# Optimization experiments

Hardware: AMD Instinct MI355X
Metric: run time of the kernel (lower is better)

## Reference

```python
import jax, jax.numpy as jnp
import numpy as np

N_NODES = 50000
N_EDGES = 800000
D_IN = 64
D_OUT = 64

def setup_inputs() -> dict:
    key = jax.random.key(0)
    k1, k2, k3, k4 = jax.random.split(key, 4)
    x = jax.random.normal(k1, (N_NODES, D_IN), dtype=jnp.float32)
    # Linear(in, out, bias=False): weight shape [out, in], Kaiming-uniform-ish scale
    bound = 1.0 / np.sqrt(D_IN)
    W = jax.random.uniform(k2, (D_OUT, D_IN), dtype=jnp.float32, minval=-bound, maxval=bound)
    src = jax.random.randint(k3, (N_EDGES,), 0, N_NODES, dtype=jnp.int32)
    dst = jax.random.randint(k4, (N_EDGES,), 0, N_NODES, dtype=jnp.int32)
    return {"x": x, "W": W, "src": src, "dst": dst}

def reference(x, W, src, dst):
    # update_all(copy_src, sum): for each edge (s, d), add x[s] into node d
    agg = jax.ops.segment_sum(x[src], dst, num_segments=N_NODES)  # [N, D_IN]
    # linear1 (bias=False); dropout is identity at inference
    h = jnp.einsum('nd,od->no', agg, W)  # [N, D_OUT]
    h = jax.nn.relu(h)
    # is_normalize=False -> skip L2 normalize; residual adds input node features
    return h + x
```

## Files before the change

kernel.cpp:

```cpp
#include <hip/hip_runtime.h>

#define D 64
#define NCHUNK 256
#define GEMMB 1024
#define CAP 48

__device__ __forceinline__ float bflo(unsigned u) { return __uint_as_float(u << 16); }
__device__ __forceinline__ float bfhi(unsigned u) { return __uint_as_float(u & 0xffff0000u); }
__device__ __forceinline__ unsigned short f2bf(float f) {
    unsigned b = __float_as_uint(f);
    return (unsigned short)((b + 0x7fffu + ((b >> 16) & 1u)) >> 16);
}

__global__ __launch_bounds__(256) void hist_kernel(
    const int* __restrict__ dst, unsigned int* __restrict__ bh32, int n_nodes, int ne) {
    __shared__ unsigned int lds[12544];
    const int tid = threadIdx.x;
    const int nw = (n_nodes + 3) >> 2;
    const int c = blockIdx.x;
    const int csz = (ne + NCHUNK - 1) / NCHUNK;
    const int e0 = c * csz, e1 = min(e0 + csz, ne);
    for (int i = tid; i < nw; i += 256) lds[i] = 0;
    __syncthreads();
    for (int e = e0 + tid; e < e1; e += 256) {
        const int d = dst[e];
        atomicAdd(&lds[d >> 2], 1u << ((d & 3) * 8));
    }
    __syncthreads();
    unsigned int* bh = bh32 + (size_t)c * nw;
    for (int i = tid; i < nw; i += 256) bh[i] = lds[i];
}

__global__ __launch_bounds__(256) void colscan_gemm_kernel(
    const float* __restrict__ x, const float* __restrict__ W,
    unsigned char* __restrict__ bh8, int* __restrict__ counts,
    unsigned short* __restrict__ ybf, int n_nodes, int ne, int csb) {
    __shared__ float lds[5184];
    const int tid = threadIdx.x;
    if ((int)blockIdx.x < csb) {
        const int d = blockIdx.x * 256 + tid;
        if (d >= n_nodes) return;
        const size_t npad4 = (size_t)((n_nodes + 3) >> 2) * 4;
        int acc = 0;
        for (int c0 = 0; c0 < NCHUNK; c0 += 8) {
            unsigned char v[8];
#pragma unroll
            for (int k = 0; k < 8; ++k) v[k] = bh8[(size_t)(c0 + k) * npad4 + d];
#pragma unroll
            for (int k = 0; k < 8; ++k) {
                bh8[(size_t)(c0 + k) * npad4 + d] = (unsigned char)acc;
                acc += v[k];
            }
        }
        counts[d] = acc;
    } else {
        float* Wt = lds;
        float* As = Wt + 64 * 65;
        for (int i = tid; i < 4096; i += 256) {
            const int o = i >> 6, k = i & 63;
            Wt[k * 65 + o] = W[i];
        }
        const int w = tid >> 6, o = tid & 63;
        const float4* x4 = (const float4*)x;
        const int ngrp = (n_nodes + 15) >> 4;
        for (int grp = blockIdx.x - csb; grp < ngrp; grp += GEMMB) {
            const int base = grp * 16;
            __syncthreads();
            const int idx = base * 16 + tid;
            if (idx < n_nodes * 16) ((float4*)As)[tid] = x4[idx];
            __syncthreads();
            const float* a0 = &As[(w * 4 + 0) * 64];
            const float* a1 = &As[(w * 4 + 1) * 64];
            const float* a2 = &As[(w * 4 + 2) * 64];
            const float* a3 = &As[(w * 4 + 3) * 64];
            float h0 = 0.f, h1 = 0.f, h2 = 0.f, h3 = 0.f;
#pragma unroll
            for (int k = 0; k < 64; ++k) {
                const float wv = Wt[k * 65 + o];
                h0 = fmaf(a0[k], wv, h0);
                h1 = fmaf(a1[k], wv, h1);
                h2 = fmaf(a2[k], wv, h2);
                h3 = fmaf(a3[k], wv, h3);
            }
            const int n0 = base + w * 4;
            if (n0 + 3 < n_nodes) {
                ybf[(size_t)(n0 + 0) * D + o] = f2bf(h0);
                ybf[(size_t)(n0 + 1) * D + o] = f2bf(h1);
                ybf[(size_t)(n0 + 2) * D + o] = f2bf(h2);
                ybf[(size_t)(n0 + 3) * D + o] = f2bf(h3);
            } else {
                if (n0 + 0 < n_nodes) ybf[(size_t)(n0 + 0) * D + o] = f2bf(h0);
                if (n0 + 1 < n_nodes) ybf[(size_t)(n0 + 1) * D + o] = f2bf(h1);
                if (n0 + 2 < n_nodes) ybf[(size_t)(n0 + 2) * D + o] = f2bf(h2);
                if (n0 + 3 < n_nodes) ybf[(size_t)(n0 + 3) * D + o] = f2bf(h3);
            }
        }
    }
}

__global__ __launch_bounds__(256) void place_kernel(
    const int* __restrict__ src, const int* __restrict__ dst,
    const unsigned int* __restrict__ bh32, int* __restrict__ esrc,
    int n_nodes, int ne) {
    __shared__ unsigned int lw[12544];
    const int c = blockIdx.x;
    const int csz = (ne + NCHUNK - 1) / NCHUNK;
    const int e0 = c * csz, e1 = min(e0 + csz, ne);
    const int nw = (n_nodes + 3) >> 2;
    const unsigned int* bh = bh32 + (size_t)c * nw;
    for (int i = threadIdx.x; i < nw; i += 256) lw[i] = bh[i];
    __syncthreads();
    for (int e = e0 + threadIdx.x; e < e1; e += 256) {
        const int d = dst[e];
        const unsigned old = atomicAdd(&lw[d >> 2], 1u << ((d & 3) * 8));
        const int slot = (old >> ((d & 3) * 8)) & 0xff;
        if (slot < CAP) esrc[d * CAP + slot] = src[e];
    }
}

__global__ void gather_kernel(const int* __restrict__ counts, const int* __restrict__ esrc,
                              const unsigned short* __restrict__ ybf,
                              const float* __restrict__ x, float* __restrict__ out,
                              int n_nodes) {
    const int tid = threadIdx.x;
    const int w = tid >> 6, lane = tid & 63;
    const int g = lane >> 3, m = lane & 7;
    const uint4* Y4 = (const uint4*)ybf;
    const float4* x4 = (const float4*)x;
    float4* out4 = (float4*)out;
    const int nWaves = gridDim.x * 4;

    int n = blockIdx.x * 4 + w;
    int c = 0, s_all = 0;
    if (n < n_nodes) {
        c = min(counts[n], CAP);
        s_all = (lane < c) ? esrc[n * CAP + lane] : 0;
    }
    while (n < n_nodes) {
        const int n2 = n + nWaves;
        int c2 = 0, s2 = 0;
        if (n2 < n_nodes) {
            c2 = min(counts[n2], CAP);
            s2 = (lane < c2) ? esrc[n2 * CAP + lane] : 0;
        }
        float acc[8] = {0.f, 0.f, 0.f, 0.f, 0.f, 0.f, 0.f, 0.f};
        for (int j = 0; j < c; j += 8) {
            const int e = j + g;
            const int s = __shfl(s_all, e);
            if (e < c) {
                const uint4 v = Y4[(size_t)s * 8 + m];
                acc[0] += bflo(v.x); acc[1] += bfhi(v.x);
                acc[2] += bflo(v.y); acc[3] += bfhi(v.y);
                acc[4] += bflo(v.z); acc[5] += bfhi(v.z);
                acc[6] += bflo(v.w); acc[7] += bfhi(v.w);
            }
        }
#pragma unroll
        for (int k = 0; k < 8; ++k) {
            acc[k] += __shfl_xor(acc[k], 8);
            acc[k] += __shfl_xor(acc[k], 16);
            acc[k] += __shfl_xor(acc[k], 32);
        }
        if (lane < 8) {
            const float4 xa = x4[(size_t)n * 16 + lane * 2];
            const float4 xb = x4[(size_t)n * 16 + lane * 2 + 1];
            float4 oa, ob;
            oa.x = fmaxf(acc[0], 0.f) + xa.x;
            oa.y = fmaxf(acc[1], 0.f) + xa.y;
            oa.z = fmaxf(acc[2], 0.f) + xa.z;
            oa.w = fmaxf(acc[3], 0.f) + xa.w;
            ob.x = fmaxf(acc[4], 0.f) + xb.x;
            ob.y = fmaxf(acc[5], 0.f) + xb.y;
            ob.z = fmaxf(acc[6], 0.f) + xb.z;
            ob.w = fmaxf(acc[7], 0.f) + xb.w;
            out4[(size_t)n * 16 + lane * 2] = oa;
            out4[(size_t)n * 16 + lane * 2 + 1] = ob;
        }
        n = n2; c = c2; s_all = s2;
    }
}

extern "C" void kernel_launch(void* const* d_in, const int* in_sizes, int n_in,
                              void* d_out, int out_size, void* d_ws, size_t ws_size,
                              hipStream_t stream) {
    const float* x = (const float*)d_in[0];
    const float* W = (const float*)d_in[1];
    const int* src = (const int*)d_in[2];
    const int* dst = (const int*)d_in[3];
    float* out = (float*)d_out;

    const int n_nodes = in_sizes[0] / D;
    const int n_edges = in_sizes[2];
    const int nw = (n_nodes + 3) >> 2;

    unsigned int* bh32 = (unsigned int*)d_ws;
    int* counts = (int*)(bh32 + (size_t)NCHUNK * nw);
    int* esrc = counts + n_nodes;
    unsigned short* ybf = (unsigned short*)(esrc + (size_t)n_nodes * CAP);

    const int csb = (n_nodes + 255) / 256;

    hist_kernel<<<NCHUNK, 256, 0, stream>>>(dst, bh32, n_nodes, n_edges);
    colscan_gemm_kernel<<<csb + GEMMB, 256, 0, stream>>>(
        x, W, (unsigned char*)bh32, counts, ybf, n_nodes, n_edges, csb);
    place_kernel<<<NCHUNK, 256, 0, stream>>>(src, dst, bh32, esrc, n_nodes, n_edges);
    gather_kernel<<<2048, 256, 0, stream>>>(counts, esrc, ybf, x, out, n_nodes);
}
```

Baseline: 136.2 us.

## Replace chunked histogram counting sort with global atomic slot assignment

Removes the per-chunk LDS histogram kernel and the column prefix scan, and replaces them with a zeroing pass fused into the GEMM kernel plus a per-edge global atomicAdd on node counters to pick each edge's bucket slot. This eliminates a kernel launch and the large per-chunk histogram buffer traffic. In exchange, edge order within each node becomes nondeterministic and global atomics may contend on popular nodes.

Result: slower. 153.9 us (+13.0%).

```diff
diff --git a/kernel.cpp b/kernel.cpp
--- a/kernel.cpp
+++ b/kernel.cpp
@@ -1,8 +1,8 @@
 #include <hip/hip_runtime.h>
 
 #define D 64
-#define NCHUNK 256
 #define GEMMB 1024
+#define ZB 32
 #define CAP 48
 
 __device__ __forceinline__ float bflo(unsigned u) { return __uint_as_float(u << 16); }
@@ -12,110 +12,66 @@
     return (unsigned short)((b + 0x7fffu + ((b >> 16) & 1u)) >> 16);
 }
 
-__global__ __launch_bounds__(256) void hist_kernel(
-    const int* __restrict__ dst, unsigned int* __restrict__ bh32, int n_nodes, int ne) {
-    __shared__ unsigned int lds[12544];
-    const int tid = threadIdx.x;
-    const int nw = (n_nodes + 3) >> 2;
-    const int c = blockIdx.x;
-    const int csz = (ne + NCHUNK - 1) / NCHUNK;
-    const int e0 = c * csz, e1 = min(e0 + csz, ne);
-    for (int i = tid; i < nw; i += 256) lds[i] = 0;
-    __syncthreads();
-    for (int e = e0 + tid; e < e1; e += 256) {
-        const int d = dst[e];
-        atomicAdd(&lds[d >> 2], 1u << ((d & 3) * 8));
-    }
-    __syncthreads();
-    unsigned int* bh = bh32 + (size_t)c * nw;
-    for (int i = tid; i < nw; i += 256) bh[i] = lds[i];
-}
-
-__global__ __launch_bounds__(256) void colscan_gemm_kernel(
+__global__ __launch_bounds__(256) void zero_gemm_kernel(
     const float* __restrict__ x, const float* __restrict__ W,
-    unsigned char* __restrict__ bh8, int* __restrict__ counts,
-    unsigned short* __restrict__ ybf, int n_nodes, int ne, int csb) {
+    int* __restrict__ counts, unsigned short* __restrict__ ybf, int n_nodes) {
     __shared__ float lds[5184];
     const int tid = threadIdx.x;
-    if ((int)blockIdx.x < csb) {
-        const int d = blockIdx.x * 256 + tid;
-        if (d >= n_nodes) return;
-        const size_t npad4 = (size_t)((n_nodes + 3) >> 2) * 4;
-        int acc = 0;
-        for (int c0 = 0; c0 < NCHUNK; c0 += 8) {
-            unsigned char v[8];
+    if ((int)blockIdx.x < ZB) {
+        for (int i = blockIdx.x * 256 + tid; i < n_nodes; i += ZB * 256) counts[i] = 0;
+        return;
+    }
+    float* Wt = lds;
+    float* As = Wt + 64 * 65;
+    for (int i = tid; i < 4096; i += 256) {
+        const int o = i >> 6, k = i & 63;
+        Wt[k * 65 + o] = W[i];
+    }
+    const int w = tid >> 6, o = tid & 63;
+    const float4* x4 = (const float4*)x;
+    const int ngrp = (n_nodes + 15) >> 4;
+    for (int grp = blockIdx.x - ZB; grp < ngrp; grp += GEMMB) {
+        const int base = grp * 16;
+        __syncthreads();
+        const int idx = base * 16 + tid;
+        if (idx < n_nodes * 16) ((float4*)As)[tid] = x4[idx];
+        __syncthreads();
+        const float* a0 = &As[(w * 4 + 0) * 64];
+        const float* a1 = &As[(w * 4 + 1) * 64];
+        const float* a2 = &As[(w * 4 + 2) * 64];
+        const float* a3 = &As[(w * 4 + 3) * 64];
+        float h0 = 0.f, h1 = 0.f, h2 = 0.f, h3 = 0.f;
 #pragma unroll
-            for (int k = 0; k < 8; ++k) v[k] = bh8[(size_t)(c0 + k) * npad4 + d];
-#pragma unroll
-            for (int k = 0; k < 8; ++k) {
-                bh8[(size_t)(c0 + k) * npad4 + d] = (unsigned char)acc;
-                acc += v[k];
-            }
+        for (int k = 0; k < 64; ++k) {
+            const float wv = Wt[k * 65 + o];
+            h0 = fmaf(a0[k], wv, h0);
+            h1 = fmaf(a1[k], wv, h1);
+            h2 = fmaf(a2[k], wv, h2);
+            h3 = fmaf(a3[k], wv, h3);
         }
-        counts[d] = acc;
-    } else {
-        float* Wt = lds;
-        float* As = Wt + 64 * 65;
-        for (int i = tid; i < 4096; i += 256) {
-            const int o = i >> 6, k = i & 63;
-            Wt[k * 65 + o] = W[i];
-        }
-        const int w = tid >> 6, o = tid & 63;
-        const float4* x4 = (const float4*)x;
-        const int ngrp = (n_nodes + 15) >> 4;
-        for (int grp = blockIdx.x - csb; grp < ngrp; grp += GEMMB) {
-            const int base = grp * 16;
-            __syncthreads();
-            const int idx = base * 16 + tid;
-            if (idx < n_nodes * 16) ((float4*)As)[tid] = x4[idx];
-            __syncthreads();
-            const float* a0 = &As[(w * 4 + 0) * 64];
-            const float* a1 = &As[(w * 4 + 1) * 64];
-            const float* a2 = &As[(w * 4 + 2) * 64];
-            const float* a3 = &As[(w * 4 + 3) * 64];
-            float h0 = 0.f, h1 = 0.f, h2 = 0.f, h3 = 0.f;
-#pragma unroll
-            for (int k = 0; k < 64; ++k) {
-                const float wv = Wt[k * 65 + o];
-                h0 = fmaf(a0[k], wv, h0);
-                h1 = fmaf(a1[k], wv, h1);
-                h2 = fmaf(a2[k], wv, h2);
-                h3 = fmaf(a3[k], wv, h3);
-            }
-            const int n0 = base + w * 4;
-            if (n0 + 3 < n_nodes) {
-                ybf[(size_t)(n0 + 0) * D + o] = f2bf(h0);
-                ybf[(size_t)(n0 + 1) * D + o] = f2bf(h1);
-                ybf[(size_t)(n0 + 2) * D + o] = f2bf(h2);
-                ybf[(size_t)(n0 + 3) * D + o] = f2bf(h3);
-            } else {
-                if (n0 + 0 < n_nodes) ybf[(size_t)(n0 + 0) * D + o] = f2bf(h0);
-                if (n0 + 1 < n_nodes) ybf[(size_t)(n0 + 1) * D + o] = f2bf(h1);
-                if (n0 + 2 < n_nodes) ybf[(size_t)(n0 + 2) * D + o] = f2bf(h2);
-                if (n0 + 3 < n_nodes) ybf[(size_t)(n0 + 3) * D + o] = f2bf(h3);
-            }
+        const int n0 = base + w * 4;
+        if (n0 + 3 < n_nodes) {
+            ybf[(size_t)(n0 + 0) * D + o] = f2bf(h0);
+            ybf[(size_t)(n0 + 1) * D + o] = f2bf(h1);
+            ybf[(size_t)(n0 + 2) * D + o] = f2bf(h2);
+            ybf[(size_t)(n0 + 3) * D + o] = f2bf(h3);
+        } else {
+            if (n0 + 0 < n_nodes) ybf[(size_t)(n0 + 0) * D + o] = f2bf(h0);
+            if (n0 + 1 < n_nodes) ybf[(size_t)(n0 + 1) * D + o] = f2bf(h1);
+            if (n0 + 2 < n_nodes) ybf[(size_t)(n0 + 2) * D + o] = f2bf(h2);
+            if (n0 + 3 < n_nodes) ybf[(size_t)(n0 + 3) * D + o] = f2bf(h3);
         }
     }
 }
 
 __global__ __launch_bounds__(256) void place_kernel(
     const int* __restrict__ src, const int* __restrict__ dst,
-    const unsigned int* __restrict__ bh32, int* __restrict__ esrc,
-    int n_nodes, int ne) {
-    __shared__ unsigned int lw[12544];
-    const int c = blockIdx.x;
-    const int csz = (ne + NCHUNK - 1) / NCHUNK;
-    const int e0 = c * csz, e1 = min(e0 + csz, ne);
-    const int nw = (n_nodes + 3) >> 2;
-    const unsigned int* bh = bh32 + (size_t)c * nw;
-    for (int i = threadIdx.x; i < nw; i += 256) lw[i] = bh[i];
-    __syncthreads();
-    for (int e = e0 + threadIdx.x; e < e1; e += 256) {
-        const int d = dst[e];
-        const unsigned old = atomicAdd(&lw[d >> 2], 1u << ((d & 3) * 8));
-        const int slot = (old >> ((d & 3) * 8)) & 0xff;
-        if (slot < CAP) esrc[d * CAP + slot] = src[e];
-    }
+    int* __restrict__ counts, int* __restrict__ esrc, int ne) {
+    const int e = blockIdx.x * 256 + threadIdx.x;
+    if (e >= ne) return;
+    const int d = dst[e];
+    const int slot = atomicAdd(&counts[d], 1);
+    if (slot < CAP) esrc[d * CAP + slot] = src[e];
 }
 
 __global__ void gather_kernel(const int* __restrict__ counts, const int* __restrict__ esrc,
@@ -191,18 +147,12 @@
 
     const int n_nodes = in_sizes[0] / D;
     const int n_edges = in_sizes[2];
-    const int nw = (n_nodes + 3) >> 2;
 
-    unsigned int* bh32 = (unsigned int*)d_ws;
-    int* counts = (int*)(bh32 + (size_t)NCHUNK * nw);
+    int* counts = (int*)d_ws;
     int* esrc = counts + n_nodes;
     unsigned short* ybf = (unsigned short*)(esrc + (size_t)n_nodes * CAP);
 
-    const int csb = (n_nodes + 255) / 256;
-
-    hist_kernel<<<NCHUNK, 256, 0, stream>>>(dst, bh32, n_nodes, n_edges);
-    colscan_gemm_kernel<<<csb + GEMMB, 256, 0, stream>>>(
-        x, W, (unsigned char*)bh32, counts, ybf, n_nodes, n_edges, csb);
-    place_kernel<<<NCHUNK, 256, 0, stream>>>(src, dst, bh32, esrc, n_nodes, n_edges);
+    zero_gemm_kernel<<<ZB + GEMMB, 256, 0, stream>>>(x, W, counts, ybf, n_nodes);
+    place_kernel<<<(n_edges + 255) / 256, 256, 0, stream>>>(src, dst, counts, esrc, n_edges);
     gather_kernel<<<2048, 256, 0, stream>>>(counts, esrc, ybf, x, out, n_nodes);
 }
```

## Register-tile the pre-GEMM with 4x4 outputs per thread and swizzled LDS

Applied to the files above, without the earlier changes.

Rewrites the GEMM branch of the colscan/gemm kernel. Each block now handles 64 rows, each thread computes a 4x4 output tile using float4 LDS reads, and the x tile is stored with an XOR swizzle to avoid bank conflicts. The grid-stride loop over 16-row groups is replaced by one block per 64-row group, which launches far more blocks. This cuts LDS traffic per FMA, but every block now reloads W into LDS and the output stores are strided bf16 writes.

Result: faster. 131.9 us (-3.2%).

```diff
diff --git a/kernel.cpp b/kernel.cpp
--- a/kernel.cpp
+++ b/kernel.cpp
@@ -2,7 +2,6 @@
 
 #define D 64
 #define NCHUNK 256
-#define GEMMB 1024
 #define CAP 48
 
 __device__ __forceinline__ float bflo(unsigned u) { return __uint_as_float(u << 16); }
@@ -35,7 +34,7 @@
     const float* __restrict__ x, const float* __restrict__ W,
     unsigned char* __restrict__ bh8, int* __restrict__ counts,
     unsigned short* __restrict__ ybf, int n_nodes, int ne, int csb) {
-    __shared__ float lds[5184];
+    __shared__ float4 lds4[2048];
     const int tid = threadIdx.x;
     if ((int)blockIdx.x < csb) {
         const int d = blockIdx.x * 256 + tid;
@@ -53,48 +52,58 @@
             }
         }
         counts[d] = acc;
-    } else {
-        float* Wt = lds;
-        float* As = Wt + 64 * 65;
-        for (int i = tid; i < 4096; i += 256) {
-            const int o = i >> 6, k = i & 63;
-            Wt[k * 65 + o] = W[i];
-        }
-        const int w = tid >> 6, o = tid & 63;
-        const float4* x4 = (const float4*)x;
-        const int ngrp = (n_nodes + 15) >> 4;
-        for (int grp = blockIdx.x - csb; grp < ngrp; grp += GEMMB) {
-            const int base = grp * 16;
-            __syncthreads();
-            const int idx = base * 16 + tid;
-            if (idx < n_nodes * 16) ((float4*)As)[tid] = x4[idx];
-            __syncthreads();
-            const float* a0 = &As[(w * 4 + 0) * 64];
-            const float* a1 = &As[(w * 4 + 1) * 64];
-            const float* a2 = &As[(w * 4 + 2) * 64];
-            const float* a3 = &As[(w * 4 + 3) * 64];
-            float h0 = 0.f, h1 = 0.f, h2 = 0.f, h3 = 0.f;
-#pragma unroll
-            for (int k = 0; k < 64; ++k) {
-                const float wv = Wt[k * 65 + o];
-                h0 = fmaf(a0[k], wv, h0);
-                h1 = fmaf(a1[k], wv, h1);
-                h2 = fmaf(a2[k], wv, h2);
-                h3 = fmaf(a3[k], wv, h3);
+        return;
+    }
+    float4* As4 = lds4;
+    float4* Wc4 = lds4 + 1024;
+    const float4* W4 = (const float4*)W;
+    for (int i = tid; i < 1024; i += 256) {
+        const int kc = i >> 6, o = i & 63;
+        Wc4[i] = W4[o * 16 + kc];
+    }
+    const int grp = (int)blockIdx.x - csb;
+    const int base = grp * 64;
+    const float4* x4 = (const float4*)x;
+#pragma unroll
+    for (int r = 0; r < 4; ++r) {
+        const int i = r * 256 + tid;
+        const int row = i >> 4, col = i & 15;
+        const int gidx = base * 16 + i;
+        if (gidx < n_nodes * 16) As4[row * 16 + (col ^ (row & 15))] = x4[gidx];
+    }
+    __syncthreads();
+    const int q = tid & 15, g = tid >> 4;
+    float acc[4][4];
+#pragma unroll
+    for (int j = 0; j < 4; ++j)
+#pragma unroll
+        for (int i = 0; i < 4; ++i) acc[j][i] = 0.f;
+    for (int kc = 0; kc < 16; ++kc) {
+        float4 a[4], wv[4];
+#pragma unroll
+        for (int j = 0; j < 4; ++j) {
+            const int rr = g * 4 + j;
+            a[j] = As4[rr * 16 + (kc ^ (rr & 15))];
+        }
+#pragma unroll
+        for (int i = 0; i < 4; ++i) wv[i] = Wc4[kc * 64 + q + 16 * i];
+#pragma unroll
+        for (int j = 0; j < 4; ++j)
+#pragma unroll
+            for (int i = 0; i < 4; ++i) {
+                acc[j][i] = fmaf(a[j].x, wv[i].x, acc[j][i]);
+                acc[j][i] = fmaf(a[j].y, wv[i].y, acc[j][i]);
+                acc[j][i] = fmaf(a[j].z, wv[i].z, acc[j][i]);
+                acc[j][i] = fmaf(a[j].w, wv[i].w, acc[j][i]);
             }
-            const int n0 = base + w * 4;
-            if (n0 + 3 < n_nodes) {
-                ybf[(size_t)(n0 + 0) * D + o] = f2bf(h0);
-                ybf[(size_t)(n0 + 1) * D + o] = f2bf(h1);
-                ybf[(size_t)(n0 + 2) * D + o] = f2bf(h2);
-                ybf[(size_t)(n0 + 3) * D + o] = f2bf(h3);
-            } else {
-                if (n0 + 0 < n_nodes) ybf[(size_t)(n0 + 0) * D + o] = f2bf(h0);
-                if (n0 + 1 < n_nodes) ybf[(size_t)(n0 + 1) * D + o] = f2bf(h1);
-                if (n0 + 2 < n_nodes) ybf[(size_t)(n0 + 2) * D + o] = f2bf(h2);
-                if (n0 + 3 < n_nodes) ybf[(size_t)(n0 + 3) * D + o] = f2bf(h3);
-            }
-        }
+    }
+#pragma unroll
+    for (int j = 0; j < 4; ++j) {
+        const int n = base + g * 4 + j;
+        if (n >= n_nodes) break;
+#pragma unroll
+        for (int i = 0; i < 4; ++i)
+            ybf[(size_t)n * D + q + 16 * i] = f2bf(acc[j][i]);
     }
 }
 
@@ -199,9 +208,10 @@
     unsigned short* ybf = (unsigned short*)(esrc + (size_t)n_nodes * CAP);
 
     const int csb = (n_nodes + 255) / 256;
+    const int ngrp = (n_nodes + 63) / 64;
 
     hist_kernel<<<NCHUNK, 256, 0, stream>>>(dst, bh32, n_nodes, n_edges);
-    colscan_gemm_kernel<<<csb + GEMMB, 256, 0, stream>>>(
+    colscan_gemm_kernel<<<csb + ngrp, 256, 0, stream>>>(
         x, W, (unsigned char*)bh32, counts, ybf, n_nodes, n_edges, csb);
     place_kernel<<<NCHUNK, 256, 0, stream>>>(src, dst, bh32, esrc, n_nodes, n_edges);
     gather_kernel<<<2048, 256, 0, stream>>>(counts, esrc, ybf, x, out, n_nodes);
```
